# Performance work log

Measured on AMD Instinct MI355X. Metric: run time of the kernel, lower is better.

## Reference

```python
import jax, jax.numpy as jnp
import numpy as np

# ---- model constants (match init_kwargs) ----
B, N = 128, 4096                 # N_BATCH, N_NEURON
N_STEPS, N_STEADY, N_WINDOW = 200, 100, 20
V_THRESH, V_REST = 1.0, 0.0
DT, TAU, TAU_SYN = 0.01, 0.02, 0.02
EXP_DT_TAU = float(np.exp(-DT / TAU))
DT_TAU = DT / TAU
EXP_DT_TAU_SYN = float(np.exp(-DT / TAU_SYN))
DT_TAU_SYN = DT / TAU_SYN

# recording schedule: steps >= N_STEADY with step % N_WINDOW == 0
REC_IDX = np.arange(N_STEADY, N_STEPS, N_WINDOW)                     # [100,120,140,160,180]
PREV_IDX = np.concatenate([[N_STEADY - N_WINDOW - 1], REC_IDX[:-1]])  # window starts (exclusive)


def setup_inputs() -> dict:
    key = jax.random.key(0)
    k1, k2, k3 = jax.random.split(key, 3)
    # feedforward drive with a positive baseline so the net actually spikes
    ff_input = 0.5 + 0.3 * jax.random.normal(k1, (B, N_STEPS, N), jnp.float32)
    # recurrent weights (transposed, as in torch: spikes @ Wab_T)
    Wab_T = jax.random.normal(k2, (N, N), jnp.float32) / np.sqrt(N)
    # initial synaptic recurrent input (torch initVolt uses randn)
    rec0 = jax.random.normal(k3, (B, N), jnp.float32)
    return {"ff_input": ff_input, "Wab_T": Wab_T, "rec0": rec0}


def reference(ff_input, Wab_T, rec0):
    dtype = ff_input.dtype
    volts0 = jnp.zeros((B, N), dtype)
    spikes0 = jnp.zeros((B, N), dtype)  # volts=0 < V_THRESH -> no initial spikes

    def step(carry, ff_t):
        volts, rec, spikes = carry
        hidden = spikes @ Wab_T                              # [B,N] GEMM
        rec = rec * EXP_DT_TAU_SYN + hidden * DT_TAU_SYN     # synaptic decay (SYN_DYN)
        volts = volts * EXP_DT_TAU + DT_TAU * (ff_t + rec)   # LIF voltage update
        spk = volts >= V_THRESH
        volts = jnp.where(spk, V_REST, volts)                # masked reset
        spikes = spk.astype(dtype)
        return (volts, rec, spikes), (spikes, volts)

    _, (spk_all, v_all) = jax.lax.scan(
        step, (volts0, rec0, spikes0), jnp.swapaxes(ff_input, 0, 1)
    )  # spk_all, v_all: [N_STEPS, B, N]

    # windowed moving averages, matching torch accumulate/reset logic
    cs_s = jnp.cumsum(spk_all, axis=0)
    cs_v = jnp.cumsum(v_all, axis=0)
    rates = (cs_s[REC_IDX] - cs_s[PREV_IDX]) / N_WINDOW      # [5, B, N]
    volts_avg = (cs_v[REC_IDX] - cs_v[PREV_IDX]) / N_WINDOW
    spikes_rec = spk_all[REC_IDX]

    return (
        jnp.swapaxes(rates, 0, 1),       # [B, 5, N]
        jnp.swapaxes(volts_avg, 0, 1),   # [B, 5, N]
        jnp.swapaxes(spikes_rec, 0, 1),  # [B, 5, N]
    )
```

## Files before the change

### kernel.cpp

```cpp
#include <hip/hip_runtime.h>
#include <stdint.h>

#define NBATCH 128
#define NNEUR  4096
#define TLAST  180
#define DECAY  0.6065306597126334f

__global__ __launch_bounds__(256) void lif_step(
    const float* __restrict__ ff, const float* __restrict__ W,
    const float* __restrict__ rec0, float* __restrict__ out,
    float* __restrict__ volts, float* __restrict__ rec,
    float* __restrict__ sum_s, float* __restrict__ sum_v,
    const unsigned long long* __restrict__ bits_old,
    unsigned long long* __restrict__ bits_new, int t)
{
#pragma clang fp contract(off)
    __shared__ unsigned short slist[NNEUR];
    __shared__ int scnt;

    const int tid  = threadIdx.x;
    const int lane = tid & 63;
    const int wid  = tid >> 6;
    const int bid  = blockIdx.x;
    const int b    = bid >> 2;
    const int c0   = ((bid & 3) << 10) + (wid << 8);
    const int n0   = c0 + (lane << 2);

    float4 acc = make_float4(0.f, 0.f, 0.f, 0.f);

    if (t > 0) {
        if (wid == 0) {
            unsigned long long m = bits_old[(b << 6) + lane];
            int c = __popcll(m);
            int x = c;
            #pragma unroll
            for (int o = 1; o < 64; o <<= 1) {
                int y = __shfl_up(x, (unsigned)o);
                if (lane >= o) x += y;
            }
            if (lane == 63) scnt = x;
            int widx = x - c;
            const int jb = ((lane >> 2) << 8) + (lane & 3);
            while (m) {
                int u = __builtin_ctzll(m);
                m &= m - 1;
                slist[widx++] = (unsigned short)(jb + (u << 2));
            }
        }
        __syncthreads();

        const int cnt = scnt;
        const float* wbase = W + n0;
        #pragma unroll 4
        for (int i = 0; i < cnt; ++i) {
            const int j = slist[i];
            const float4 wv = *(const float4*)(wbase + ((size_t)j << 12));
            acc.x += wv.x; acc.y += wv.y; acc.z += wv.z; acc.w += wv.w;
        }
    }

    const size_t idx = ((size_t)b << 12) + (size_t)n0;

    float4 r4 = (t == 0) ? *(const float4*)(rec0 + idx)
                         : *(const float4*)(rec + idx);
    r4.x = r4.x * DECAY + acc.x * 0.5f;
    r4.y = r4.y * DECAY + acc.y * 0.5f;
    r4.z = r4.z * DECAY + acc.z * 0.5f;
    r4.w = r4.w * DECAY + acc.w * 0.5f;

    const float4 f4 = *(const float4*)(ff + (((size_t)b * 200 + (size_t)t) << 12) + n0);

    float4 v4 = make_float4(0.f, 0.f, 0.f, 0.f);
    if (t > 0) v4 = *(const float4*)(volts + idx);
    v4.x = v4.x * DECAY + 0.5f * (f4.x + r4.x);
    v4.y = v4.y * DECAY + 0.5f * (f4.y + r4.y);
    v4.z = v4.z * DECAY + 0.5f * (f4.z + r4.z);
    v4.w = v4.w * DECAY + 0.5f * (f4.w + r4.w);

    const bool s0 = v4.x >= 1.0f, s1 = v4.y >= 1.0f, s2 = v4.z >= 1.0f, s3 = v4.w >= 1.0f;
    if (s0) v4.x = 0.f;
    if (s1) v4.y = 0.f;
    if (s2) v4.z = 0.f;
    if (s3) v4.w = 0.f;

    *(float4*)(volts + idx) = v4;
    *(float4*)(rec + idx)   = r4;

    const unsigned long long b0 = __ballot(s0), b1 = __ballot(s1),
                             b2 = __ballot(s2), b3 = __ballot(s3);
    if (lane == 0) {
        unsigned long long* dst = bits_new + (b << 6) + (c0 >> 6);
        dst[0] = b0; dst[1] = b1; dst[2] = b2; dst[3] = b3;
    }

    if (t >= 80) {
        const float4 s4 = make_float4(s0 ? 1.f : 0.f, s1 ? 1.f : 0.f,
                                      s2 ? 1.f : 0.f, s3 ? 1.f : 0.f);
        const bool start = (t == 80) || (t == 101) || (t == 121) || (t == 141) || (t == 161);
        float4 ss, sv;
        if (start) {
            ss = s4; sv = v4;
        } else {
            ss = *(const float4*)(sum_s + idx);
            sv = *(const float4*)(sum_v + idx);
            ss.x += s4.x; ss.y += s4.y; ss.z += s4.z; ss.w += s4.w;
            sv.x += v4.x; sv.y += v4.y; sv.z += v4.z; sv.w += v4.w;
        }
        *(float4*)(sum_s + idx) = ss;
        *(float4*)(sum_v + idx) = sv;

        if (t >= 100 && ((t - 100) % 20) == 0) {
            const int k = (t - 100) / 20;
            const size_t oidx = (((size_t)b * 5 + (size_t)k) << 12) + n0;
            float* rates = out;
            float* vavg  = out + (size_t)NBATCH * 5 * NNEUR;
            float* srec  = out + (size_t)NBATCH * 5 * NNEUR * 2;
            *(float4*)(rates + oidx) = make_float4(ss.x / 20.f, ss.y / 20.f,
                                                   ss.z / 20.f, ss.w / 20.f);
            *(float4*)(vavg + oidx)  = make_float4(sv.x / 20.f, sv.y / 20.f,
                                                   sv.z / 20.f, sv.w / 20.f);
            *(float4*)(srec + oidx)  = s4;
        }
    }
}

extern "C" void kernel_launch(void* const* d_in, const int* in_sizes, int n_in,
                              void* d_out, int out_size, void* d_ws, size_t ws_size,
                              hipStream_t stream) {
    const float* ff   = (const float*)d_in[0];
    const float* W    = (const float*)d_in[1];
    const float* rec0 = (const float*)d_in[2];
    float* out = (float*)d_out;

    char* ws = (char*)d_ws;
    const size_t STATE = (size_t)NBATCH * NNEUR * sizeof(float);
    float* volts = (float*)(ws);
    float* rec   = (float*)(ws + STATE);
    float* sum_s = (float*)(ws + 2 * STATE);
    float* sum_v = (float*)(ws + 3 * STATE);
    unsigned long long* bits = (unsigned long long*)(ws + 4 * STATE);
    const int BWORDS = NBATCH * (NNEUR / 64);

    for (int t = 0; t <= TLAST; ++t) {
        lif_step<<<dim3(512), dim3(256), 0, stream>>>(
            ff, W, rec0, out, volts, rec, sum_s, sum_v,
            bits + (size_t)(t & 1) * BWORDS,
            bits + (size_t)((t + 1) & 1) * BWORDS, t);
    }
}
```

Baseline: 3.642 ms.

## Halve per-thread width, double grid, and software-pipeline scalarized weight gathers

Each thread now handles two neurons with float2 instead of four with float4, and the grid doubles to 1024 blocks, giving more waves in flight for the sparse weight-row gather. The spike bitmask layout and the decode into the spike list are changed to match the new lane-to-neuron mapping. The gather loop reads eight spike indices per LDS vector load and makes them wave-uniform with readfirstlane. It also double-buffers eight loads ahead of accumulation to hide memory latency. The cost is more, smaller 8-byte loads per row, more blocks each rebuilding the spike list, and higher register use from the load buffers.

```diff
diff --git a/kernel.cpp b/kernel.cpp
--- a/kernel.cpp
+++ b/kernel.cpp
@@ -15,18 +15,20 @@
     unsigned long long* __restrict__ bits_new, int t)
 {
 #pragma clang fp contract(off)
-    __shared__ unsigned short slist[NNEUR];
+    __shared__ __align__(16) unsigned short slist[NNEUR];
     __shared__ int scnt;
 
     const int tid  = threadIdx.x;
     const int lane = tid & 63;
     const int wid  = tid >> 6;
     const int bid  = blockIdx.x;
-    const int b    = bid >> 2;
-    const int c0   = ((bid & 3) << 10) + (wid << 8);
-    const int n0   = c0 + (lane << 2);
+    const int b    = bid >> 3;
+    const int tile = bid & 7;
+    const int c0   = (tile << 9) + (wid << 7);
+    const int n0   = c0 + (lane << 1);
+    const unsigned laneb = (unsigned)n0 * 4u;
 
-    float4 acc = make_float4(0.f, 0.f, 0.f, 0.f);
+    float accx = 0.f, accy = 0.f;
 
     if (t > 0) {
         if (wid == 0) {
@@ -40,74 +42,95 @@
             }
             if (lane == 63) scnt = x;
             int widx = x - c;
-            const int jb = ((lane >> 2) << 8) + (lane & 3);
+            const int jb = ((lane >> 1) << 7) + (lane & 1);
             while (m) {
                 int u = __builtin_ctzll(m);
                 m &= m - 1;
-                slist[widx++] = (unsigned short)(jb + (u << 2));
+                slist[widx++] = (unsigned short)(jb + (u << 1));
             }
         }
         __syncthreads();
 
         const int cnt = scnt;
-        const float* wbase = W + n0;
-        #pragma unroll 4
-        for (int i = 0; i < cnt; ++i) {
-            const int j = slist[i];
-            const float4 wv = *(const float4*)(wbase + ((size_t)j << 12));
-            acc.x += wv.x; acc.y += wv.y; acc.z += wv.z; acc.w += wv.w;
+        const char* Wb = (const char*)W;
+
+        auto load8 = [&](float2* R, int ii) {
+            const uint4 pk = *(const uint4*)(slist + ii);
+            unsigned q[4];
+            q[0] = pk.x; q[1] = pk.y; q[2] = pk.z; q[3] = pk.w;
+            #pragma unroll
+            for (int k = 0; k < 4; ++k) {
+                const unsigned qq = __builtin_amdgcn_readfirstlane(q[k]);
+                R[2 * k]     = *(const float2*)(Wb + (((qq & 0xffffu) << 14) + laneb));
+                R[2 * k + 1] = *(const float2*)(Wb + (((qq >> 16)     << 14) + laneb));
+            }
+        };
+        auto acc8 = [&](const float2* R) {
+            #pragma unroll
+            for (int k = 0; k < 8; ++k) { accx += R[k].x; accy += R[k].y; }
+        };
+
+        int i = 0;
+        if (cnt >= 8) {
+            float2 A[8], B[8];
+            load8(A, 0); i = 8;
+            while (i + 16 <= cnt) {
+                load8(B, i);     acc8(A);
+                load8(A, i + 8); acc8(B);
+                i += 16;
+            }
+            if (i + 8 <= cnt) { load8(B, i); acc8(A); acc8(B); i += 8; }
+            else              { acc8(A); }
+        }
+        for (; i < cnt; ++i) {
+            unsigned q = (unsigned)slist[i];
+            q = __builtin_amdgcn_readfirstlane(q);
+            const float2 w = *(const float2*)(Wb + ((q << 14) + laneb));
+            accx += w.x; accy += w.y;
         }
     }
 
     const size_t idx = ((size_t)b << 12) + (size_t)n0;
 
-    float4 r4 = (t == 0) ? *(const float4*)(rec0 + idx)
-                         : *(const float4*)(rec + idx);
-    r4.x = r4.x * DECAY + acc.x * 0.5f;
-    r4.y = r4.y * DECAY + acc.y * 0.5f;
-    r4.z = r4.z * DECAY + acc.z * 0.5f;
-    r4.w = r4.w * DECAY + acc.w * 0.5f;
+    float2 r2 = (t == 0) ? *(const float2*)(rec0 + idx)
+                         : *(const float2*)(rec + idx);
+    r2.x = r2.x * DECAY + accx * 0.5f;
+    r2.y = r2.y * DECAY + accy * 0.5f;
 
-    const float4 f4 = *(const float4*)(ff + (((size_t)b * 200 + (size_t)t) << 12) + n0);
+    const float2 f2 = *(const float2*)(ff + (((size_t)b * 200 + (size_t)t) << 12) + n0);
 
-    float4 v4 = make_float4(0.f, 0.f, 0.f, 0.f);
-    if (t > 0) v4 = *(const float4*)(volts + idx);
-    v4.x = v4.x * DECAY + 0.5f * (f4.x + r4.x);
-    v4.y = v4.y * DECAY + 0.5f * (f4.y + r4.y);
-    v4.z = v4.z * DECAY + 0.5f * (f4.z + r4.z);
-    v4.w = v4.w * DECAY + 0.5f * (f4.w + r4.w);
+    float2 v2 = make_float2(0.f, 0.f);
+    if (t > 0) v2 = *(const float2*)(volts + idx);
+    v2.x = v2.x * DECAY + 0.5f * (f2.x + r2.x);
+    v2.y = v2.y * DECAY + 0.5f * (f2.y + r2.y);
 
-    const bool s0 = v4.x >= 1.0f, s1 = v4.y >= 1.0f, s2 = v4.z >= 1.0f, s3 = v4.w >= 1.0f;
-    if (s0) v4.x = 0.f;
-    if (s1) v4.y = 0.f;
-    if (s2) v4.z = 0.f;
-    if (s3) v4.w = 0.f;
+    const bool s0 = v2.x >= 1.0f, s1 = v2.y >= 1.0f;
+    if (s0) v2.x = 0.f;
+    if (s1) v2.y = 0.f;
 
-    *(float4*)(volts + idx) = v4;
-    *(float4*)(rec + idx)   = r4;
+    *(float2*)(volts + idx) = v2;
+    *(float2*)(rec + idx)   = r2;
 
-    const unsigned long long b0 = __ballot(s0), b1 = __ballot(s1),
-                             b2 = __ballot(s2), b3 = __ballot(s3);
+    const unsigned long long m0 = __ballot(s0), m1 = __ballot(s1);
     if (lane == 0) {
-        unsigned long long* dst = bits_new + (b << 6) + (c0 >> 6);
-        dst[0] = b0; dst[1] = b1; dst[2] = b2; dst[3] = b3;
+        unsigned long long* dst = bits_new + (b << 6) + ((c0 >> 7) << 1);
+        dst[0] = m0; dst[1] = m1;
     }
 
     if (t >= 80) {
-        const float4 s4 = make_float4(s0 ? 1.f : 0.f, s1 ? 1.f : 0.f,
-                                      s2 ? 1.f : 0.f, s3 ? 1.f : 0.f);
+        const float2 s2 = make_float2(s0 ? 1.f : 0.f, s1 ? 1.f : 0.f);
         const bool start = (t == 80) || (t == 101) || (t == 121) || (t == 141) || (t == 161);
-        float4 ss, sv;
+        float2 ss, sv;
         if (start) {
-            ss = s4; sv = v4;
+            ss = s2; sv = v2;
         } else {
-            ss = *(const float4*)(sum_s + idx);
-            sv = *(const float4*)(sum_v + idx);
-            ss.x += s4.x; ss.y += s4.y; ss.z += s4.z; ss.w += s4.w;
-            sv.x += v4.x; sv.y += v4.y; sv.z += v4.z; sv.w += v4.w;
+            ss = *(const float2*)(sum_s + idx);
+            sv = *(const float2*)(sum_v + idx);
+            ss.x += s2.x; ss.y += s2.y;
+            sv.x += v2.x; sv.y += v2.y;
         }
-        *(float4*)(sum_s + idx) = ss;
-        *(float4*)(sum_v + idx) = sv;
+        *(float2*)(sum_s + idx) = ss;
+        *(float2*)(sum_v + idx) = sv;
 
         if (t >= 100 && ((t - 100) % 20) == 0) {
             const int k = (t - 100) / 20;
@@ -115,11 +138,9 @@
             float* rates = out;
             float* vavg  = out + (size_t)NBATCH * 5 * NNEUR;
             float* srec  = out + (size_t)NBATCH * 5 * NNEUR * 2;
-            *(float4*)(rates + oidx) = make_float4(ss.x / 20.f, ss.y / 20.f,
-                                                   ss.z / 20.f, ss.w / 20.f);
-            *(float4*)(vavg + oidx)  = make_float4(sv.x / 20.f, sv.y / 20.f,
-                                                   sv.z / 20.f, sv.w / 20.f);
-            *(float4*)(srec + oidx)  = s4;
+            *(float2*)(rates + oidx) = make_float2(ss.x / 20.f, ss.y / 20.f);
+            *(float2*)(vavg  + oidx) = make_float2(sv.x / 20.f, sv.y / 20.f);
+            *(float2*)(srec  + oidx) = s2;
         }
     }
 }
@@ -142,7 +163,7 @@
     const int BWORDS = NBATCH * (NNEUR / 64);
 
     for (int t = 0; t <= TLAST; ++t) {
-        lif_step<<<dim3(512), dim3(256), 0, stream>>>(
+        lif_step<<<dim3(1024), dim3(256), 0, stream>>>(
             ff, W, rec0, out, volts, rec, sum_s, sum_v,
             bits + (size_t)(t & 1) * BWORDS,
             bits + (size_t)((t + 1) & 1) * BWORDS, t);
```

After: 3.721 ms. 1.02x slower.

## Fuse all timesteps into one persistent kernel with per-batch spin barriers

Applied to the files above, without the earlier changes.

Replaces 181 per-timestep kernel launches with a single persistent kernel. The four blocks that share a batch row synchronise each step through an atomic counter and flag barrier. Voltage, synaptic and window-sum state now live in registers instead of global memory, which removes per-step state loads and stores as well as launch overhead. The cost is spin-waiting, and the design relies on all 512 blocks being co-resident (launch bounds of 2 blocks per SM); otherwise it deadlocks.

```diff
diff --git a/kernel.cpp b/kernel.cpp
--- a/kernel.cpp
+++ b/kernel.cpp
@@ -5,14 +5,18 @@
 #define NNEUR  4096
 #define TLAST  180
 #define DECAY  0.6065306597126334f
+#define SCOPE  __HIP_MEMORY_SCOPE_AGENT
 
-__global__ __launch_bounds__(256) void lif_step(
+__global__ void lif_init(unsigned* cnt, unsigned* flag) {
+    const int i = threadIdx.x;
+    if (i < NBATCH) { cnt[i] = 0u; flag[i] = 0u; }
+}
+
+__global__ __launch_bounds__(256, 2) void lif_persist(
     const float* __restrict__ ff, const float* __restrict__ W,
     const float* __restrict__ rec0, float* __restrict__ out,
-    float* __restrict__ volts, float* __restrict__ rec,
-    float* __restrict__ sum_s, float* __restrict__ sum_v,
-    const unsigned long long* __restrict__ bits_old,
-    unsigned long long* __restrict__ bits_new, int t)
+    unsigned long long* __restrict__ bits,
+    unsigned* __restrict__ cnt, unsigned* __restrict__ flag)
 {
 #pragma clang fp contract(off)
     __shared__ unsigned short slist[NNEUR];
@@ -23,103 +27,123 @@
     const int wid  = tid >> 6;
     const int bid  = blockIdx.x;
     const int b    = bid >> 2;
-    const int c0   = ((bid & 3) << 10) + (wid << 8);
+    const int tile = bid & 3;
+    const int c0   = (tile << 10) + (wid << 8);
     const int n0   = c0 + (lane << 2);
 
-    float4 acc = make_float4(0.f, 0.f, 0.f, 0.f);
+    const float* wbase = W + n0;
+    const float* fptr  = ff + (((size_t)b * 200) << 12) + n0;
+    const size_t idx   = ((size_t)b << 12) + (size_t)n0;
 
-    if (t > 0) {
-        if (wid == 0) {
-            unsigned long long m = bits_old[(b << 6) + lane];
-            int c = __popcll(m);
-            int x = c;
-            #pragma unroll
-            for (int o = 1; o < 64; o <<= 1) {
-                int y = __shfl_up(x, (unsigned)o);
-                if (lane >= o) x += y;
+    float4 v4 = make_float4(0.f, 0.f, 0.f, 0.f);
+    float4 r4 = *(const float4*)(rec0 + idx);
+    float4 ss = v4, sv = v4;
+    unsigned tgt = 0;
+
+    for (int t = 0; t <= TLAST; ++t) {
+        const float4 f4 = *(const float4*)fptr;
+        fptr += NNEUR;
+
+        float4 acc = make_float4(0.f, 0.f, 0.f, 0.f);
+        if (t > 0) {
+            const unsigned long long* bsrc =
+                bits + (((size_t)((t - 1) & 1)) << 13) + (b << 6);
+            if (wid == 0) {
+                unsigned long long m =
+                    __hip_atomic_load(&bsrc[lane], __ATOMIC_RELAXED, SCOPE);
+                const int c = __popcll(m);
+                int x = c;
+                #pragma unroll
+                for (int o = 1; o < 64; o <<= 1) {
+                    int y = __shfl_up(x, (unsigned)o);
+                    if (lane >= o) x += y;
+                }
+                if (lane == 63) scnt = x;
+                int widx = x - c;
+                const int jb = ((lane >> 2) << 8) + (lane & 3);
+                while (m) {
+                    const int u = __builtin_ctzll(m);
+                    m &= m - 1;
+                    slist[widx++] = (unsigned short)(jb + (u << 2));
+                }
             }
-            if (lane == 63) scnt = x;
-            int widx = x - c;
-            const int jb = ((lane >> 2) << 8) + (lane & 3);
-            while (m) {
-                int u = __builtin_ctzll(m);
-                m &= m - 1;
-                slist[widx++] = (unsigned short)(jb + (u << 2));
+            __syncthreads();
+
+            const int cn = scnt;
+            #pragma unroll 4
+            for (int i = 0; i < cn; ++i) {
+                const int j = slist[i];
+                const float4 wv = *(const float4*)(wbase + ((size_t)j << 12));
+                acc.x += wv.x; acc.y += wv.y; acc.z += wv.z; acc.w += wv.w;
             }
         }
-        __syncthreads();
 
-        const int cnt = scnt;
-        const float* wbase = W + n0;
-        #pragma unroll 4
-        for (int i = 0; i < cnt; ++i) {
-            const int j = slist[i];
-            const float4 wv = *(const float4*)(wbase + ((size_t)j << 12));
-            acc.x += wv.x; acc.y += wv.y; acc.z += wv.z; acc.w += wv.w;
+        r4.x = r4.x * DECAY + acc.x * 0.5f;
+        r4.y = r4.y * DECAY + acc.y * 0.5f;
+        r4.z = r4.z * DECAY + acc.z * 0.5f;
+        r4.w = r4.w * DECAY + acc.w * 0.5f;
+
+        v4.x = v4.x * DECAY + 0.5f * (f4.x + r4.x);
+        v4.y = v4.y * DECAY + 0.5f * (f4.y + r4.y);
+        v4.z = v4.z * DECAY + 0.5f * (f4.z + r4.z);
+        v4.w = v4.w * DECAY + 0.5f * (f4.w + r4.w);
+
+        const bool s0 = v4.x >= 1.0f, s1 = v4.y >= 1.0f,
+                   s2 = v4.z >= 1.0f, s3 = v4.w >= 1.0f;
+        if (s0) v4.x = 0.f;
+        if (s1) v4.y = 0.f;
+        if (s2) v4.z = 0.f;
+        if (s3) v4.w = 0.f;
+
+        const unsigned long long m0 = __ballot(s0), m1 = __ballot(s1),
+                                 m2 = __ballot(s2), m3 = __ballot(s3);
+        if (t < TLAST && lane == 0) {
+            unsigned long long* dst =
+                bits + (((size_t)(t & 1)) << 13) + (b << 6) + (c0 >> 6);
+            __hip_atomic_store(&dst[0], m0, __ATOMIC_RELAXED, SCOPE);
+            __hip_atomic_store(&dst[1], m1, __ATOMIC_RELAXED, SCOPE);
+            __hip_atomic_store(&dst[2], m2, __ATOMIC_RELAXED, SCOPE);
+            __hip_atomic_store(&dst[3], m3, __ATOMIC_RELAXED, SCOPE);
         }
-    }
 
-    const size_t idx = ((size_t)b << 12) + (size_t)n0;
+        if (t >= 80) {
+            const float4 s4 = make_float4(s0 ? 1.f : 0.f, s1 ? 1.f : 0.f,
+                                          s2 ? 1.f : 0.f, s3 ? 1.f : 0.f);
+            const bool start = (t == 80) || (t == 101) || (t == 121) ||
+                               (t == 141) || (t == 161);
+            if (start) {
+                ss = s4; sv = v4;
+            } else {
+                ss.x += s4.x; ss.y += s4.y; ss.z += s4.z; ss.w += s4.w;
+                sv.x += v4.x; sv.y += v4.y; sv.z += v4.z; sv.w += v4.w;
+            }
+            if (t == 100 || t == 120 || t == 140 || t == 160 || t == 180) {
+                const int k = (t - 100) / 20;
+                const size_t oidx = (((size_t)b * 5 + (size_t)k) << 12) + n0;
+                float* rates = out;
+                float* vavg  = out + (size_t)NBATCH * 5 * NNEUR;
+                float* srec  = out + (size_t)NBATCH * 5 * NNEUR * 2;
+                *(float4*)(rates + oidx) = make_float4(ss.x / 20.f, ss.y / 20.f,
+                                                       ss.z / 20.f, ss.w / 20.f);
+                *(float4*)(vavg + oidx)  = make_float4(sv.x / 20.f, sv.y / 20.f,
+                                                       sv.z / 20.f, sv.w / 20.f);
+                *(float4*)(srec + oidx)  = s4;
+            }
+        }
 
-    float4 r4 = (t == 0) ? *(const float4*)(rec0 + idx)
-                         : *(const float4*)(rec + idx);
-    r4.x = r4.x * DECAY + acc.x * 0.5f;
-    r4.y = r4.y * DECAY + acc.y * 0.5f;
-    r4.z = r4.z * DECAY + acc.z * 0.5f;
-    r4.w = r4.w * DECAY + acc.w * 0.5f;
-
-    const float4 f4 = *(const float4*)(ff + (((size_t)b * 200 + (size_t)t) << 12) + n0);
-
-    float4 v4 = make_float4(0.f, 0.f, 0.f, 0.f);
-    if (t > 0) v4 = *(const float4*)(volts + idx);
-    v4.x = v4.x * DECAY + 0.5f * (f4.x + r4.x);
-    v4.y = v4.y * DECAY + 0.5f * (f4.y + r4.y);
-    v4.z = v4.z * DECAY + 0.5f * (f4.z + r4.z);
-    v4.w = v4.w * DECAY + 0.5f * (f4.w + r4.w);
-
-    const bool s0 = v4.x >= 1.0f, s1 = v4.y >= 1.0f, s2 = v4.z >= 1.0f, s3 = v4.w >= 1.0f;
-    if (s0) v4.x = 0.f;
-    if (s1) v4.y = 0.f;
-    if (s2) v4.z = 0.f;
-    if (s3) v4.w = 0.f;
-
-    *(float4*)(volts + idx) = v4;
-    *(float4*)(rec + idx)   = r4;
-
-    const unsigned long long b0 = __ballot(s0), b1 = __ballot(s1),
-                             b2 = __ballot(s2), b3 = __ballot(s3);
-    if (lane == 0) {
-        unsigned long long* dst = bits_new + (b << 6) + (c0 >> 6);
-        dst[0] = b0; dst[1] = b1; dst[2] = b2; dst[3] = b3;
-    }
-
-    if (t >= 80) {
-        const float4 s4 = make_float4(s0 ? 1.f : 0.f, s1 ? 1.f : 0.f,
-                                      s2 ? 1.f : 0.f, s3 ? 1.f : 0.f);
-        const bool start = (t == 80) || (t == 101) || (t == 121) || (t == 141) || (t == 161);
-        float4 ss, sv;
-        if (start) {
-            ss = s4; sv = v4;
-        } else {
-            ss = *(const float4*)(sum_s + idx);
-            sv = *(const float4*)(sum_v + idx);
-            ss.x += s4.x; ss.y += s4.y; ss.z += s4.z; ss.w += s4.w;
-            sv.x += v4.x; sv.y += v4.y; sv.z += v4.z; sv.w += v4.w;
-        }
-        *(float4*)(sum_s + idx) = ss;
-        *(float4*)(sum_v + idx) = sv;
-
-        if (t >= 100 && ((t - 100) % 20) == 0) {
-            const int k = (t - 100) / 20;
-            const size_t oidx = (((size_t)b * 5 + (size_t)k) << 12) + n0;
-            float* rates = out;
-            float* vavg  = out + (size_t)NBATCH * 5 * NNEUR;
-            float* srec  = out + (size_t)NBATCH * 5 * NNEUR * 2;
-            *(float4*)(rates + oidx) = make_float4(ss.x / 20.f, ss.y / 20.f,
-                                                   ss.z / 20.f, ss.w / 20.f);
-            *(float4*)(vavg + oidx)  = make_float4(sv.x / 20.f, sv.y / 20.f,
-                                                   sv.z / 20.f, sv.w / 20.f);
-            *(float4*)(srec + oidx)  = s4;
+        if (t < TLAST) {
+            ++tgt;
+            if (tid == 0) {
+                const unsigned pos =
+                    __hip_atomic_fetch_add(&cnt[b], 1u, __ATOMIC_ACQ_REL, SCOPE);
+                if (pos == 3u) {
+                    __hip_atomic_store(&cnt[b], 0u, __ATOMIC_RELAXED, SCOPE);
+                    __hip_atomic_fetch_add(&flag[b], 1u, __ATOMIC_RELEASE, SCOPE);
+                } else {
+                    while (__hip_atomic_load(&flag[b], __ATOMIC_ACQUIRE, SCOPE) < tgt) {}
+                }
+            }
+            __syncthreads();
         }
     }
 }
@@ -133,18 +157,11 @@
     float* out = (float*)d_out;
 
     char* ws = (char*)d_ws;
-    const size_t STATE = (size_t)NBATCH * NNEUR * sizeof(float);
-    float* volts = (float*)(ws);
-    float* rec   = (float*)(ws + STATE);
-    float* sum_s = (float*)(ws + 2 * STATE);
-    float* sum_v = (float*)(ws + 3 * STATE);
-    unsigned long long* bits = (unsigned long long*)(ws + 4 * STATE);
-    const int BWORDS = NBATCH * (NNEUR / 64);
+    unsigned long long* bits = (unsigned long long*)ws;
+    unsigned* cnt  = (unsigned*)(ws + 2 * 8192 * sizeof(unsigned long long));
+    unsigned* flag = cnt + NBATCH;
 
-    for (int t = 0; t <= TLAST; ++t) {
-        lif_step<<<dim3(512), dim3(256), 0, stream>>>(
-            ff, W, rec0, out, volts, rec, sum_s, sum_v,
-            bits + (size_t)(t & 1) * BWORDS,
-            bits + (size_t)((t + 1) & 1) * BWORDS, t);
-    }
+    lif_init<<<dim3(1), dim3(128), 0, stream>>>(cnt, flag);
+    lif_persist<<<dim3(512), dim3(256), 0, stream>>>(ff, W, rec0, out,
+                                                     bits, cnt, flag);
 }
```

New measurement: 8.832 ms. +142.5%, slower.
